# Optimization experiments

Hardware: AMD Instinct MI355X
Metric: run time of the kernel (lower is better)

Reference implementation:

```python
import jax, jax.numpy as jnp
import numpy as np

K = 11          # k_size in the original module
HALF = K // 2   # 5
N_SIGNAL = 33554432  # 2**25 elements, 128 MB fp32


def setup_inputs() -> dict:
    key = jax.random.key(0)
    k1, _ = jax.random.split(key)
    x = jax.random.normal(k1, (N_SIGNAL,), dtype=jnp.float32)
    # learned parameter of Dilation1D(s=1.5)
    scale = jnp.asarray(1.5, dtype=jnp.float32)
    return {"x": x, "scale": scale}


def reference(x, scale):
    # parabolic structuring element: z = -5..5, h = -z^2 / (4*scale)
    z = jnp.linspace(-(K // 2), K // 2, K, dtype=jnp.float32)  # torch: -k//2+1 .. k//2 == -5..5
    h = -(z * z) / (4.0 * scale)  # [K]

    n = x.shape[0]
    pad = jnp.full((HALF,), -jnp.inf, dtype=x.dtype)
    xp = jnp.concatenate([pad, x, pad])  # [n + K - 1], -inf edge handling == original branches

    # out[r] = max_j ( x[r - HALF + j] + h[j] )  (max-plus / grayscale dilation)
    out = xp[0:n] + h[0]
    for j in range(1, K):  # fixed small K, unrolled window — no data-dim loop
        out = jnp.maximum(out, xp[j:j + n] + h[j])
    return out
```

## Files before the change

### kernel.cpp

```cpp
#include <hip/hip_runtime.h>
#include <math.h>


#define BLOCK   256
#define QPT     4
#define TILE_Q  (BLOCK * QPT)
#define HALO_Q  2
#define STAGE_Q (TILE_Q + 2 * HALO_Q)

__global__ __launch_bounds__(BLOCK) void dilate1d_kernel(
    const float4* __restrict__ x4,
    const float*  __restrict__ scale_p,
    float4*       __restrict__ out4,
    int n4)
{
    __shared__ float4 smem[STAGE_Q];

    const float NEG  = -INFINITY;
    const float4 NEG4 = make_float4(NEG, NEG, NEG, NEG);

    const int Q0 = blockIdx.x * TILE_Q;
    const int g0 = Q0 - HALO_Q;

    const bool interior = (g0 >= 0) && (g0 + STAGE_Q <= n4);
    if (interior) {
#pragma unroll
        for (int t = 0; t < QPT; ++t) {
            int idx = threadIdx.x + t * BLOCK;
            smem[idx] = x4[g0 + idx];
        }
        if (threadIdx.x < 2 * HALO_Q) {
            int idx = TILE_Q + threadIdx.x;
            smem[idx] = x4[g0 + idx];
        }
    } else {
#pragma unroll
        for (int t = 0; t <= QPT; ++t) {
            int idx = threadIdx.x + t * BLOCK;
            if (idx < STAGE_Q) {
                int g = g0 + idx;
                smem[idx] = (g >= 0 && g < n4) ? x4[g] : NEG4;
            }
        }
    }
    __syncthreads();

    const float r4s = 1.0f / (4.0f * scale_p[0]);
    float hparr[6];
    hparr[0] = 0.0f;
    hparr[1] = -1.0f  * r4s;
    hparr[2] = -4.0f  * r4s;
    hparr[3] = -9.0f  * r4s;
    hparr[4] = -16.0f * r4s;
    hparr[5] = -25.0f * r4s;

#pragma unroll
    for (int t = 0; t < QPT; ++t) {
        int idx = threadIdx.x + t * BLOCK;
        int q   = Q0 + idx;
        if (q >= n4) break;

        float w[20];
#pragma unroll
        for (int r = 0; r < 5; ++r) {
            float4 v = smem[idx + r];
            w[4 * r + 0] = v.x;
            w[4 * r + 1] = v.y;
            w[4 * r + 2] = v.z;
            w[4 * r + 3] = v.w;
        }

        float4 o;
        float* op = &o.x;
#pragma unroll
        for (int i = 0; i < 4; ++i) {
            int c = 8 + i;
            float m = w[c];
#pragma unroll
            for (int d = 1; d <= 5; ++d) {
                m = fmaxf(m, hparr[d] + fmaxf(w[c - d], w[c + d]));
            }
            op[i] = m;
        }
        out4[q] = o;
    }
}

extern "C" void kernel_launch(void* const* d_in, const int* in_sizes, int n_in,
                              void* d_out, int out_size, void* d_ws, size_t ws_size,
                              hipStream_t stream) {
    const float* x       = (const float*)d_in[0];
    const float* scale_p = (const float*)d_in[1];
    float*       out     = (float*)d_out;

    int n  = in_sizes[0];
    int n4 = n / 4;

    int grid = (n4 + TILE_Q - 1) / TILE_Q;

    dilate1d_kernel<<<grid, BLOCK, 0, stream>>>(
        (const float4*)x, scale_p, (float4*)out, n4);
}
```

Measured before the change: 232.6 us.

## Replace shared-memory staging with per-wave overlapping tiles and lane shuffles

Removes the LDS tile and __syncthreads. Each wavefront instead loads overlapping 64-float4 tiles directly into registers and gets the neighbouring values through __shfl_up/__shfl_down, with 60 useful outputs per tile and two halo lanes on each side. This avoids LDS traffic and barrier stalls. In exchange, about 6% of loads are redundant, four lanes per tile do not store, and stores are slightly misaligned relative to 64-lane boundaries.

```diff
diff --git a/kernel.cpp b/kernel.cpp
--- a/kernel.cpp
+++ b/kernel.cpp
@@ -3,86 +3,85 @@
 
 
 #define BLOCK   256
+#define WPB     (BLOCK / 64)
 #define QPT     4
-#define TILE_Q  (BLOCK * QPT)
-#define HALO_Q  2
-#define STAGE_Q (TILE_Q + 2 * HALO_Q)
+#define TQ      60
 
 __global__ __launch_bounds__(BLOCK) void dilate1d_kernel(
     const float4* __restrict__ x4,
     const float*  __restrict__ scale_p,
     float4*       __restrict__ out4,
-    int n4)
+    int n4,
+    int ntiles)
 {
-    __shared__ float4 smem[STAGE_Q];
+    const int lane = threadIdx.x & 63;
+    const int wid  = blockIdx.x * WPB + (threadIdx.x >> 6);
+    const int tau0 = wid * QPT;
+    if (tau0 >= ntiles) return;
 
-    const float NEG  = -INFINITY;
+    const float  NEG  = -INFINITY;
     const float4 NEG4 = make_float4(NEG, NEG, NEG, NEG);
 
-    const int Q0 = blockIdx.x * TILE_Q;
-    const int g0 = Q0 - HALO_Q;
-
-    const bool interior = (g0 >= 0) && (g0 + STAGE_Q <= n4);
+    float4 v[QPT];
+    const int gbase = tau0 * TQ - 2 + lane;
+    const bool interior = (tau0 > 0) && (tau0 + QPT <= ntiles) &&
+                          ((tau0 + QPT - 1) * TQ + 62 <= n4);
     if (interior) {
 #pragma unroll
-        for (int t = 0; t < QPT; ++t) {
-            int idx = threadIdx.x + t * BLOCK;
-            smem[idx] = x4[g0 + idx];
-        }
-        if (threadIdx.x < 2 * HALO_Q) {
-            int idx = TILE_Q + threadIdx.x;
-            smem[idx] = x4[g0 + idx];
-        }
+        for (int t = 0; t < QPT; ++t)
+            v[t] = x4[gbase + t * TQ];
     } else {
 #pragma unroll
-        for (int t = 0; t <= QPT; ++t) {
-            int idx = threadIdx.x + t * BLOCK;
-            if (idx < STAGE_Q) {
-                int g = g0 + idx;
-                smem[idx] = (g >= 0 && g < n4) ? x4[g] : NEG4;
-            }
+        for (int t = 0; t < QPT; ++t) {
+            int g = gbase + t * TQ;
+            v[t] = ((tau0 + t) < ntiles && g >= 0 && g < n4) ? x4[g] : NEG4;
         }
     }
-    __syncthreads();
 
     const float r4s = 1.0f / (4.0f * scale_p[0]);
-    float hparr[6];
-    hparr[0] = 0.0f;
-    hparr[1] = -1.0f  * r4s;
-    hparr[2] = -4.0f  * r4s;
-    hparr[3] = -9.0f  * r4s;
-    hparr[4] = -16.0f * r4s;
-    hparr[5] = -25.0f * r4s;
+    const float hp1 = -1.0f  * r4s;
+    const float hp2 = -4.0f  * r4s;
+    const float hp3 = -9.0f  * r4s;
+    const float hp4 = -16.0f * r4s;
+    const float hp5 = -25.0f * r4s;
+
+    const bool storelane = (lane >= 2) && (lane < 62);
 
 #pragma unroll
     for (int t = 0; t < QPT; ++t) {
-        int idx = threadIdx.x + t * BLOCK;
-        int q   = Q0 + idx;
-        if (q >= n4) break;
+        const int tau = tau0 + t;
+        if (tau >= ntiles) break;
+        const float4 c = v[t];
 
-        float w[20];
-#pragma unroll
-        for (int r = 0; r < 5; ++r) {
-            float4 v = smem[idx + r];
-            w[4 * r + 0] = v.x;
-            w[4 * r + 1] = v.y;
-            w[4 * r + 2] = v.z;
-            w[4 * r + 3] = v.w;
-        }
+        float w[14];
+        w[0]  = __shfl_up(c.w, 2);
+        w[1]  = __shfl_up(c.x, 1);
+        w[2]  = __shfl_up(c.y, 1);
+        w[3]  = __shfl_up(c.z, 1);
+        w[4]  = __shfl_up(c.w, 1);
+        w[5]  = c.x;  w[6] = c.y;  w[7] = c.z;  w[8] = c.w;
+        w[9]  = __shfl_down(c.x, 1);
+        w[10] = __shfl_down(c.y, 1);
+        w[11] = __shfl_down(c.z, 1);
+        w[12] = __shfl_down(c.w, 1);
+        w[13] = __shfl_down(c.x, 2);
 
         float4 o;
         float* op = &o.x;
 #pragma unroll
         for (int i = 0; i < 4; ++i) {
-            int c = 8 + i;
-            float m = w[c];
-#pragma unroll
-            for (int d = 1; d <= 5; ++d) {
-                m = fmaxf(m, hparr[d] + fmaxf(w[c - d], w[c + d]));
-            }
+            const int cc = 5 + i;
+            float m = w[cc];
+            m = fmaxf(m, hp1 + fmaxf(w[cc - 1], w[cc + 1]));
+            m = fmaxf(m, hp2 + fmaxf(w[cc - 2], w[cc + 2]));
+            m = fmaxf(m, hp3 + fmaxf(w[cc - 3], w[cc + 3]));
+            m = fmaxf(m, hp4 + fmaxf(w[cc - 4], w[cc + 4]));
+            m = fmaxf(m, hp5 + fmaxf(w[cc - 5], w[cc + 5]));
             op[i] = m;
         }
-        out4[q] = o;
+
+        const int q = tau * TQ + (lane - 2);
+        if (storelane && q < n4) out4[q] = o;
     }
 }
 
@@ -93,11 +92,12 @@
     const float* scale_p = (const float*)d_in[1];
     float*       out     = (float*)d_out;
 
-    int n  = in_sizes[0];
-    int n4 = n / 4;
+    int n      = in_sizes[0];
+    int n4     = n / 4;
+    int ntiles = (n4 + TQ - 1) / TQ;
+    int waves  = (ntiles + QPT - 1) / QPT;
+    int blocks = (waves + WPB - 1) / WPB;
 
-    int grid = (n4 + TILE_Q - 1) / TILE_Q;
-
-    dilate1d_kernel<<<grid, BLOCK, 0, stream>>>(
-        (const float4*)x, scale_p, (float4*)out, n4);
+    dilate1d_kernel<<<blocks, BLOCK, 0, stream>>>(
+        (const float4*)x, scale_p, (float4*)out, n4, ntiles);
 }
```

Measured after the change: 230.3 us. Within noise of the previous version (-1.0%).
